# Performance work log

Measured on AMD Instinct MI355X. Metric: run time of the kernel, lower is better.

The kernel has to match this reference:

```python
import jax, jax.numpy as jnp
import numpy as np

B, T, D, H = 32, 2048, 256, 512


def setup_inputs() -> dict:
    key = jax.random.key(0)
    k1, k2, k3, k4 = jax.random.split(key, 4)
    datamat = jax.random.normal(k1, (B, T, D), jnp.float32)
    datalens = jax.random.randint(k2, (B,), 0, T, jnp.int32)
    si = 1.0 / np.sqrt(D)
    sh = 1.0 / np.sqrt(H)
    # flax OptimizedLSTMCell: input dense has no bias, hidden dense has bias.
    Wi = jax.random.uniform(k3, (D, 4 * H), jnp.float32, -si, si)
    Wh = jax.random.uniform(k4, (H, 4 * H), jnp.float32, -sh, sh)
    b = jnp.zeros((4 * H,), jnp.float32)
    return {"datamat": datamat, "datalens": datalens, "Wi": Wi, "Wh": Wh, "b": b}


def _lstm(datamat, datalens, Wi, Wh, b):
    Bsz, Tlen, _ = datamat.shape
    Hd = Wh.shape[0]
    # Precompute input projection for all timesteps: [B,T,4H]
    x_proj = jnp.einsum('btd,dg->btg', datamat, Wi)
    c0 = jnp.zeros((Bsz, Hd), datamat.dtype)
    h0 = jnp.zeros((Bsz, Hd), datamat.dtype)

    def step(state, xg):
        c, h, lc, lh, t = state
        gates = xg + h @ Wh + b            # [B,4H], gate order i,f,g,o
        i, f, g, o = jnp.split(gates, 4, axis=-1)
        new_c = jax.nn.sigmoid(f) * c + jax.nn.sigmoid(i) * jnp.tanh(g)
        new_h = jax.nn.sigmoid(o) * jnp.tanh(new_c)
        # latch carry at the last valid step (t < seq_len), matching flax RNN
        # which selects the carry at index seq_len-1 from an unmasked scan.
        valid = (t < datalens)[:, None]
        lc = jnp.where(valid, new_c, lc)
        lh = jnp.where(valid, new_h, lh)
        return (new_c, new_h, lc, lh, t + 1), new_h

    init = (c0, h0, c0, h0, jnp.int32(0))
    (_, _, lc, lh, _), ys = jax.lax.scan(step, init, jnp.swapaxes(x_proj, 0, 1))
    return (lc, lh), jnp.swapaxes(ys, 0, 1)  # carry=(c,h), outputs [B,T,H]


def reference(datamat, datalens, Wi, Wh, b):
    return _lstm(datamat, datalens, Wi, Wh, b)
```

## Files before the change

### kernel.cpp

```cpp
#include <hip/hip_runtime.h>
#include <cstdint>

static constexpr int BATCH  = 32;
static constexpr int TLEN   = 2048;
static constexpr int DIN    = 256;
static constexpr int HDIM   = 512;
static constexpr int G4     = 2048;
static constexpr int NSLICE = 8;
static constexpr int HCB    = 64;
static constexpr int CPB    = 256;
static constexpr int NTHR   = 512;
static constexpr int NWAVE  = 8;
static constexpr int KL     = 96;
static constexpr int KL2    = 48;
static constexpr int NBLK   = BATCH * NSLICE;

typedef _Float16 h2v __attribute__((ext_vector_type(2)));

__device__ __forceinline__ uint32_t pack_f16x2(float a, float b) {
    h2v v;
    v[0] = (_Float16)a;
    v[1] = (_Float16)b;
    return __builtin_bit_cast(uint32_t, v);
}

__device__ __forceinline__ float dot2f(uint32_t w, uint32_t u, float acc) {
#if __has_builtin(__builtin_amdgcn_fdot2)
    return __builtin_amdgcn_fdot2(__builtin_bit_cast(h2v, w),
                                  __builtin_bit_cast(h2v, u), acc, false);
#else
    h2v a = __builtin_bit_cast(h2v, w);
    h2v b = __builtin_bit_cast(h2v, u);
    return acc + (float)a[0] * (float)b[0] + (float)a[1] * (float)b[1];
#endif
}

__device__ __forceinline__ float sigmoidf_(float x) {
    return 1.0f / (1.0f + __expf(-x));
}
__device__ __forceinline__ float tanhf_(float x) {
    return 1.0f - 2.0f / (1.0f + __expf(2.0f * x));
}

__global__ __launch_bounds__(NTHR, 2) void lstm_persist(
    const float* __restrict__ x, const int* __restrict__ lens,
    const float* __restrict__ Wi, const float* __restrict__ Wh,
    const float* __restrict__ bias, float* __restrict__ out,
    uint32_t* __restrict__ hT)
{
    const int bid = blockIdx.x;
    const int xcd = bid & 7;
    const int t8  = bid >> 3;
    const int b   = xcd * 4 + (t8 & 3);
    const int s   = t8 >> 2;

    const int tid = threadIdx.x;
    const int w   = tid >> 6;
    const int l   = tid & 63;

    __shared__ __align__(16) uint32_t u_lds[NWAVE][KL2];
    __shared__ float gp[2][NWAVE][CPB];

    uint32_t wgt[4][KL2];
    #pragma unroll
    for (int q = 0; q < 4; ++q) {
        const int c    = 4 * l + q;
        const int gcol = (c >> 6) * HDIM + s * HCB + (c & 63);
        #pragma unroll
        for (int m = 0; m < KL2; ++m) {
            const int k0 = KL * w + 2 * m;
            const int k1 = k0 + 1;
            const float f0 = (k0 < DIN) ? Wi[(size_t)k0 * G4 + gcol]
                                        : Wh[(size_t)(k0 - DIN) * G4 + gcol];
            const float f1 = (k1 < DIN) ? Wi[(size_t)k1 * G4 + gcol]
                                        : Wh[(size_t)(k1 - DIN) * G4 + gcol];
            wgt[q][m] = pack_f16x2(f0, f1);
        }
    }

    float c_st = 0.f, lc_st = 0.f, lh_st = 0.f;
    float b_i = 0.f, b_f = 0.f, b_g = 0.f, b_o = 0.f;
    if (tid < HCB) {
        const int col = s * HCB + tid;
        b_i = bias[col];
        b_f = bias[HDIM + col];
        b_g = bias[2 * HDIM + col];
        b_o = bias[3 * HDIM + col];
    }
    const int len_b = lens[b];

    const float* xb = x + (size_t)b * TLEN * DIN;
    float* ys = out + 2 * BATCH * HDIM;

    const int  k0     = KL * w + 2 * l;
    const bool is_stg = (l < KL2);
    const bool is_x   = is_stg && (k0 < DIN);
    const bool is_h   = is_stg && (k0 >= DIN);

    float2 xx_cur = make_float2(0.f, 0.f);
    if (is_x) xx_cur = *(const float2*)(xb + k0);

    for (int t = 0; t < TLEN; ++t) {
        if (is_x) {
            u_lds[w][l] = pack_f16x2(xx_cur.x, xx_cur.y);
        } else if (is_h) {
            const uint64_t* src = (const uint64_t*)
                (hT + (((size_t)(t & 1) * BATCH + b) * HDIM + (k0 - DIN)));
            const uint32_t tag = (uint32_t)t;
            uint64_t v;
            for (;;) {
                v = __hip_atomic_load(src, __ATOMIC_RELAXED,
                                      __HIP_MEMORY_SCOPE_AGENT);
                const uint32_t lo_tag = (uint32_t)(v >> 16) & 0xFFFFu;
                const uint32_t hi_tag = (uint32_t)(v >> 48);
                if ((lo_tag == tag) && (hi_tag == tag)) break;
            }
            u_lds[w][l] = (uint32_t)(v & 0xFFFFu) |
                          (uint32_t)((v >> 16) & 0xFFFF0000u);
        }
        if (is_x && (t + 1 < TLEN))
            xx_cur = *(const float2*)(xb + (size_t)(t + 1) * DIN + k0);

        float a0 = 0.f, a1 = 0.f, a2 = 0.f, a3 = 0.f;
        const uint4* uv = (const uint4*)&u_lds[w][0];
        #pragma unroll
        for (int m4 = 0; m4 < KL2 / 4; ++m4) {
            const uint4 uu = uv[m4];
            a0 = dot2f(wgt[0][4 * m4 + 0], uu.x, a0);
            a0 = dot2f(wgt[0][4 * m4 + 1], uu.y, a0);
            a0 = dot2f(wgt[0][4 * m4 + 2], uu.z, a0);
            a0 = dot2f(wgt[0][4 * m4 + 3], uu.w, a0);
            a1 = dot2f(wgt[1][4 * m4 + 0], uu.x, a1);
            a1 = dot2f(wgt[1][4 * m4 + 1], uu.y, a1);
            a1 = dot2f(wgt[1][4 * m4 + 2], uu.z, a1);
            a1 = dot2f(wgt[1][4 * m4 + 3], uu.w, a1);
            a2 = dot2f(wgt[2][4 * m4 + 0], uu.x, a2);
            a2 = dot2f(wgt[2][4 * m4 + 1], uu.y, a2);
            a2 = dot2f(wgt[2][4 * m4 + 2], uu.z, a2);
            a2 = dot2f(wgt[2][4 * m4 + 3], uu.w, a2);
            a3 = dot2f(wgt[3][4 * m4 + 0], uu.x, a3);
            a3 = dot2f(wgt[3][4 * m4 + 1], uu.y, a3);
            a3 = dot2f(wgt[3][4 * m4 + 2], uu.z, a3);
            a3 = dot2f(wgt[3][4 * m4 + 3], uu.w, a3);
        }
        float4 av;
        av.x = a0; av.y = a1; av.z = a2; av.w = a3;
        *(float4*)&gp[t & 1][w][4 * l] = av;

        __syncthreads();

        if (tid < HCB) {
            float si = b_i, sf = b_f, sg = b_g, so = b_o;
            #pragma unroll
            for (int ww = 0; ww < NWAVE; ++ww) {
                si += gp[t & 1][ww][tid];
                sf += gp[t & 1][ww][HCB + tid];
                sg += gp[t & 1][ww][2 * HCB + tid];
                so += gp[t & 1][ww][3 * HCB + tid];
            }
            const float ig = sigmoidf_(si);
            const float fg = sigmoidf_(sf);
            const float gg = tanhf_(sg);
            const float og = sigmoidf_(so);
            const float cn = fg * c_st + ig * gg;
            const float hn = og * tanhf_(cn);
            c_st = cn;
            if (t < len_b) { lc_st = cn; lh_st = hn; }
            const _Float16 hf = (_Float16)hn;
            const uint32_t word = ((uint32_t)(t + 1) << 16) |
                                  (uint32_t)__builtin_bit_cast(uint16_t, hf);
            __hip_atomic_store(
                &hT[((size_t)((t + 1) & 1) * BATCH + b) * HDIM + s * HCB + tid],
                word, __ATOMIC_RELAXED, __HIP_MEMORY_SCOPE_AGENT);
            ys[((size_t)b * TLEN + t) * HDIM + s * HCB + tid] = hn;
        }
    }

    if (tid < HCB) {
        out[(size_t)b * HDIM + s * HCB + tid] = lc_st;
        out[BATCH * HDIM + (size_t)b * HDIM + s * HCB + tid] = lh_st;
    }
}

extern "C" void kernel_launch(void* const* d_in, const int* in_sizes, int n_in,
                              void* d_out, int out_size, void* d_ws, size_t ws_size,
                              hipStream_t stream)
{
    const float* x    = (const float*)d_in[0];
    const int*   lens = (const int*)d_in[1];
    const float* Wi   = (const float*)d_in[2];
    const float* Wh   = (const float*)d_in[3];
    const float* bias = (const float*)d_in[4];
    float* out = (float*)d_out;

    uint32_t* hT = (uint32_t*)d_ws;
    const size_t init_bytes = (size_t)2 * BATCH * HDIM * sizeof(uint32_t);
    hipMemsetAsync(d_ws, 0, init_bytes, stream);

    hipLaunchKernelGGL(lstm_persist, dim3(NBLK), dim3(NTHR), 0, stream,
                       x, lens, Wi, Wh, bias, out, hT);
}
```

Baseline: 3.903 ms.

## Poll hidden-state flags through L2 when all slices share one XCD

Each block publishes its XCC id in a handshake array at startup and waits until all 8 slices of its batch row have checked in. If every slice of that row sits on the same XCD, the spin-wait on the tagged h words uses a global_load with sc0, meant to hit the shared L2 instead of the agent-scope path. A bounded spin count falls back to the original atomic load, so correctness does not depend on the fast path. This adds a startup handshake and relies on the block-to-XCD mapping and L2 coherence behaviour within one XCD.

```diff
diff --git a/kernel.cpp b/kernel.cpp
--- a/kernel.cpp
+++ b/kernel.cpp
@@ -14,6 +14,7 @@
 static constexpr int KL     = 96;
 static constexpr int KL2    = 48;
 static constexpr int NBLK   = BATCH * NSLICE;
+static constexpr int SC0_SPIN_MAX = 1024;
 
 typedef _Float16 h2v __attribute__((ext_vector_type(2)));
 
@@ -42,11 +43,29 @@
     return 1.0f - 2.0f / (1.0f + __expf(2.0f * x));
 }
 
+__device__ __forceinline__ uint64_t load_l2_u64(const uint64_t* p) {
+    uint64_t r;
+    asm volatile("global_load_dwordx2 %0, %1, off sc0\n\t"
+                 "s_waitcnt vmcnt(0)"
+                 : "=&v"(r) : "v"(p) : "memory");
+    return r;
+}
+
+__device__ __forceinline__ uint32_t xcc_id() {
+    return __builtin_amdgcn_s_getreg(20 | ((32 - 1) << 11)) & 0xFu;
+}
+
+__device__ __forceinline__ bool tag_ok(uint64_t v, uint32_t tag) {
+    return (((uint32_t)(v >> 16) & 0xFFFFu) == tag) &&
+           ((uint32_t)(v >> 48) == tag);
+}
+
 __global__ __launch_bounds__(NTHR, 2) void lstm_persist(
     const float* __restrict__ x, const int* __restrict__ lens,
     const float* __restrict__ Wi, const float* __restrict__ Wh,
     const float* __restrict__ bias, float* __restrict__ out,
-    uint32_t* __restrict__ hT)
+    uint32_t* __restrict__ hT,
+    uint32_t* __restrict__ hand)
 {
     const int bid = blockIdx.x;
     const int xcd = bid & 7;
@@ -78,6 +97,20 @@
         }
     }
 
+    const uint32_t xcc = xcc_id();
+    if (tid == 0)
+        __hip_atomic_store(&hand[b * NSLICE + s], 0x100u | xcc,
+                           __ATOMIC_RELAXED, __HIP_MEMORY_SCOPE_AGENT);
+    uint32_t e = 0x100u;
+    for (;;) {
+        if (l < NSLICE)
+            e = __hip_atomic_load(&hand[b * NSLICE + l], __ATOMIC_RELAXED,
+                                  __HIP_MEMORY_SCOPE_AGENT);
+        if (__all(e >= 0x100u)) break;
+    }
+    const uint32_t e0 = __shfl(e, 0);
+    bool use_sc0 = __all((l < NSLICE) ? (e == e0) : true);
+
     float c_st = 0.f, lc_st = 0.f, lh_st = 0.f;
     float b_i = 0.f, b_f = 0.f, b_g = 0.f, b_o = 0.f;
     if (tid < HCB) {
@@ -107,13 +140,21 @@
             const uint64_t* src = (const uint64_t*)
                 (hT + (((size_t)(t & 1) * BATCH + b) * HDIM + (k0 - DIN)));
             const uint32_t tag = (uint32_t)t;
-            uint64_t v;
-            for (;;) {
-                v = __hip_atomic_load(src, __ATOMIC_RELAXED,
-                                      __HIP_MEMORY_SCOPE_AGENT);
-                const uint32_t lo_tag = (uint32_t)(v >> 16) & 0xFFFFu;
-                const uint32_t hi_tag = (uint32_t)(v >> 48);
-                if ((lo_tag == tag) && (hi_tag == tag)) break;
+            uint64_t v = 0;
+            bool got = false;
+            if (use_sc0) {
+                for (int spin = 0; spin < SC0_SPIN_MAX; ++spin) {
+                    v = load_l2_u64(src);
+                    if (tag_ok(v, tag)) { got = true; break; }
+                }
+                if (!got) use_sc0 = false;
+            }
+            if (!got) {
+                for (;;) {
+                    v = __hip_atomic_load(src, __ATOMIC_RELAXED,
+                                          __HIP_MEMORY_SCOPE_AGENT);
+                    if (tag_ok(v, tag)) break;
+                }
             }
             u_lds[w][l] = (uint32_t)(v & 0xFFFFu) |
                           (uint32_t)((v >> 16) & 0xFFFF0000u);
@@ -193,10 +234,12 @@
     const float* bias = (const float*)d_in[4];
     float* out = (float*)d_out;
 
-    uint32_t* hT = (uint32_t*)d_ws;
-    const size_t init_bytes = (size_t)2 * BATCH * HDIM * sizeof(uint32_t);
+    uint32_t* hT   = (uint32_t*)d_ws;
+    uint32_t* hand = hT + 2 * BATCH * HDIM;
+    const size_t init_bytes =
+        ((size_t)2 * BATCH * HDIM + BATCH * NSLICE) * sizeof(uint32_t);
     hipMemsetAsync(d_ws, 0, init_bytes, stream);
 
     hipLaunchKernelGGL(lstm_persist, dim3(NBLK), dim3(NTHR), 0, stream,
-                       x, lens, Wi, Wh, bias, out, hT);
-}
+                       x, lens, Wi, Wh, bias, out, hT, hand);
+}
```

Result: slower. 4.354 ms (+11.6%).
